# Kernel optimization log

Measured on AMD Instinct MI355X. Metric: run time of the kernel, lower is better.

## Reference

```python
import jax, jax.numpy as jnp
import numpy as np

TEMPERATURE = 0.5
EPS = 1e-8  # torch cosine_similarity norm clamp


def setup_inputs() -> dict:
    key = jax.random.key(0)
    k1, k2, k3 = jax.random.split(key, 3)
    N, D = 4096, 256
    z_i = jax.random.normal(k1, (N, D), dtype=jnp.float32)
    z_j = jax.random.normal(k2, (N, D), dtype=jnp.float32)
    weights = jax.random.uniform(k3, (N,), dtype=jnp.float32)
    return {"z_i": z_i, "z_j": z_j, "weights": weights}


def reference(z_i, z_j, weights):
    N = z_i.shape[0]
    z = jnp.concatenate([z_i, z_j], axis=0)  # [2N, D]
    # cosine similarity via normalized matmul (same math as broadcasted F.cosine_similarity)
    norm = jnp.maximum(jnp.linalg.norm(z, axis=1, keepdims=True), EPS)
    zn = z / norm
    sim = zn @ zn.T  # [2N, 2N]
    # positives: diagonals at offsets +N and -N
    sim_ij = jnp.diagonal(sim, offset=N)
    sim_ji = jnp.diagonal(sim, offset=-N)
    positives = jnp.concatenate([sim_ij, sim_ji], axis=0)  # [2N]
    mask = 1.0 - jnp.eye(2 * N, dtype=sim.dtype)
    denominator = jnp.sum(mask * jnp.exp(sim / TEMPERATURE), axis=1)  # [2N]
    numerator = jnp.exp(positives / TEMPERATURE)
    all_losses = -jnp.log(numerator / denominator)  # [2N]
    w2 = jnp.tile(weights, 2)  # weights.repeat(2)
    loss = jnp.sum(all_losses * w2) / jnp.sum(w2)
    return loss
```

## Files before the change

### kernel.cpp

```cpp
#include <hip/hip_runtime.h>
#include <hip/hip_bf16.h>

#define PN   4096
#define PN2  8192
#define PD   256
#define TILE 128
#define BK   64
#define NBLK (PN2 / TILE)
#define NTRI (NBLK * (NBLK + 1) / 2)

typedef __attribute__((ext_vector_type(8))) short bf16x8;
typedef __attribute__((ext_vector_type(4))) float f32x4;

typedef const __attribute__((address_space(1))) void* gas_ptr;
typedef __attribute__((address_space(3))) void* las_ptr;

__global__ __launch_bounds__(256) void normalize_kernel(
    const float* __restrict__ zi, const float* __restrict__ zj,
    __hip_bfloat16* __restrict__ zn, float* __restrict__ rowsum) {
  int r = blockIdx.x;
  int tid = threadIdx.x;
  const float* src = (r < PN) ? (zi + (size_t)r * PD) : (zj + (size_t)(r - PN) * PD);
  float x = src[tid];
  float s = x * x;
  #pragma unroll
  for (int off = 32; off >= 1; off >>= 1) s += __shfl_xor(s, off, 64);
  __shared__ float p[4];
  if ((tid & 63) == 0) p[tid >> 6] = s;
  __syncthreads();
  float tot = p[0] + p[1] + p[2] + p[3];
  float nrm = fmaxf(sqrtf(tot), 1e-8f);
  zn[(size_t)r * PD + tid] = __float2bfloat16(x / nrm);
  if (tid == 0) rowsum[r] = 0.0f;
}

__global__ __launch_bounds__(256) void simsum_kernel(
    const __hip_bfloat16* __restrict__ zn,
    float* __restrict__ rowsum, float* __restrict__ pos) {
  __shared__ char lds[2 * TILE * BK * 2];
  char* As = lds;
  char* Bs = lds + TILE * BK * 2;

  const int idx = blockIdx.x;
  int bj = (int)((sqrtf(8.0f * (float)idx + 1.0f) - 1.0f) * 0.5f);
  while ((bj + 1) * (bj + 2) / 2 <= idx) ++bj;
  while (bj * (bj + 1) / 2 > idx) --bj;
  const int bi = idx - bj * (bj + 1) / 2;
  const bool diagBlk = (bi == bj);
  const bool posBlk  = (bj == bi + PN / TILE);

  const int tid  = threadIdx.x;
  const int wave = tid >> 6;
  const int lane = tid & 63;
  const int quad = lane >> 4;
  const int c16  = lane & 15;
  const int rowBase = bi * TILE;
  const int colBase = bj * TILE;
  const int waveRow = (wave >> 1) * 64;
  const int waveCol = (wave & 1) * 64;

  f32x4 acc[4][4];
  #pragma unroll
  for (int i = 0; i < 4; ++i)
    #pragma unroll
    for (int j = 0; j < 4; ++j)
      acc[i][j] = (f32x4){0.f, 0.f, 0.f, 0.f};

  const int subrow = lane >> 3;
  const int slot   = lane & 7;
  const char* BsEff = diagBlk ? As : Bs;

  for (int kt = 0; kt < PD / BK; ++kt) {
    if (kt) __syncthreads();
    #pragma unroll
    for (int p = 0; p < 4; ++p) {
      int issue = wave * 4 + p;
      int r = issue * 8 + subrow;
      int c = slot ^ (r & 7);
      const __hip_bfloat16* ga = zn + (size_t)(rowBase + r) * PD + kt * BK + c * 8;
      __builtin_amdgcn_global_load_lds((gas_ptr)ga, (las_ptr)(As + issue * 1024), 16, 0, 0);
      if (!diagBlk) {
        const __hip_bfloat16* gb = zn + (size_t)(colBase + r) * PD + kt * BK + c * 8;
        __builtin_amdgcn_global_load_lds((gas_ptr)gb, (las_ptr)(Bs + issue * 1024), 16, 0, 0);
      }
    }
    __syncthreads();

    #pragma unroll
    for (int ki = 0; ki < 2; ++ki) {
      bf16x8 a[4], b[4];
      #pragma unroll
      for (int mi = 0; mi < 4; ++mi) {
        int r = waveRow + mi * 16 + c16;
        int ch = quad + ki * 4;
        a[mi] = *(const bf16x8*)(As + r * 128 + ((ch ^ (r & 7)) * 16));
      }
      #pragma unroll
      for (int ni = 0; ni < 4; ++ni) {
        int r = waveCol + ni * 16 + c16;
        int ch = quad + ki * 4;
        b[ni] = *(const bf16x8*)(BsEff + r * 128 + ((ch ^ (r & 7)) * 16));
      }
      #pragma unroll
      for (int mi = 0; mi < 4; ++mi)
        #pragma unroll
        for (int ni = 0; ni < 4; ++ni)
          acc[mi][ni] = __builtin_amdgcn_mfma_f32_16x16x32_bf16(a[mi], b[ni], acc[mi][ni], 0, 0, 0);
    }
  }

  float colsum[4] = {0.f, 0.f, 0.f, 0.f};
  #pragma unroll
  for (int mi = 0; mi < 4; ++mi) {
    int rbase = rowBase + waveRow + mi * 16 + quad * 4;
    float rs[4] = {0.f, 0.f, 0.f, 0.f};
    #pragma unroll
    for (int ni = 0; ni < 4; ++ni) {
      int gcol = colBase + waveCol + ni * 16 + c16;
      #pragma unroll
      for (int t = 0; t < 4; ++t) {
        int grow = rbase + t;
        float sim = acc[mi][ni][t];
        float e = __expf(2.0f * sim);
        if (diagBlk && gcol == grow) e = 0.0f;
        rs[t] += e;
        colsum[ni] += e;
        if (posBlk && gcol == grow + PN) {
          pos[grow] = sim;
          pos[grow + PN] = sim;
        }
      }
    }
    #pragma unroll
    for (int t = 0; t < 4; ++t) {
      #pragma unroll
      for (int off = 1; off <= 8; off <<= 1) rs[t] += __shfl_xor(rs[t], off, 64);
    }
    if (c16 == 0) {
      #pragma unroll
      for (int t = 0; t < 4; ++t) atomicAdd(&rowsum[rbase + t], rs[t]);
    }
  }
  if (!diagBlk) {
    #pragma unroll
    for (int ni = 0; ni < 4; ++ni) {
      float cs = colsum[ni];
      cs += __shfl_xor(cs, 16, 64);
      cs += __shfl_xor(cs, 32, 64);
      if (quad == 0) atomicAdd(&rowsum[colBase + waveCol + ni * 16 + c16], cs);
    }
  }
}

__global__ __launch_bounds__(1024) void finalize_kernel(
    const float* __restrict__ rowsum, const float* __restrict__ pos,
    const float* __restrict__ w, float* __restrict__ out) {
  int tid = threadIdx.x;
  float wl = 0.f, ws = 0.f;
  for (int i = tid; i < PN2; i += 1024) {
    float li = logf(rowsum[i]) - 2.0f * pos[i];
    float wi = w[i & (PN - 1)];
    wl += wi * li;
    ws += wi;
  }
  #pragma unroll
  for (int off = 32; off >= 1; off >>= 1) {
    wl += __shfl_xor(wl, off, 64);
    ws += __shfl_xor(ws, off, 64);
  }
  __shared__ float pl[16], pw[16];
  if ((tid & 63) == 0) { pl[tid >> 6] = wl; pw[tid >> 6] = ws; }
  __syncthreads();
  if (tid == 0) {
    float sl = 0.f, sw = 0.f;
    #pragma unroll
    for (int k = 0; k < 16; ++k) { sl += pl[k]; sw += pw[k]; }
    out[0] = sl / sw;
  }
}

extern "C" void kernel_launch(void* const* d_in, const int* in_sizes, int n_in,
                              void* d_out, int out_size, void* d_ws, size_t ws_size,
                              hipStream_t stream) {
  const float* zi = (const float*)d_in[0];
  const float* zj = (const float*)d_in[1];
  const float* w  = (const float*)d_in[2];
  float* out = (float*)d_out;

  __hip_bfloat16* zn = (__hip_bfloat16*)d_ws;
  float* rowsum = (float*)((char*)d_ws + (size_t)PN2 * PD * 2);
  float* pos = rowsum + PN2;

  normalize_kernel<<<PN2, 256, 0, stream>>>(zi, zj, zn, rowsum);
  simsum_kernel<<<NTRI, 256, 0, stream>>>(zn, rowsum, pos);
  finalize_kernel<<<1, 1024, 0, stream>>>(rowsum, pos, w, out);
}
```

Baseline: 110.7 us.

## Load MFMA operands directly from global memory and vectorize normalization per wave

The similarity kernel no longer stages tiles in LDS with global_load_lds and barriers. Each lane now loads its bf16x8 MFMA fragments straight from global memory into registers, double-buffered across the eight K-steps. This removes LDS traffic and __syncthreads, but every wave re-reads rows that other waves in the block share, so it relies on L1/L2 cache hits. The normalize kernel is also changed to one wave per row with float4 loads and packed bf16 stores, which drops the shared-memory reduction.

```diff
diff --git a/kernel.cpp b/kernel.cpp
--- a/kernel.cpp
+++ b/kernel.cpp
@@ -5,42 +5,36 @@
 #define PN2  8192
 #define PD   256
 #define TILE 128
-#define BK   64
 #define NBLK (PN2 / TILE)
 #define NTRI (NBLK * (NBLK + 1) / 2)
 
 typedef __attribute__((ext_vector_type(8))) short bf16x8;
 typedef __attribute__((ext_vector_type(4))) float f32x4;
 
-typedef const __attribute__((address_space(1))) void* gas_ptr;
-typedef __attribute__((address_space(3))) void* las_ptr;
-
 __global__ __launch_bounds__(256) void normalize_kernel(
     const float* __restrict__ zi, const float* __restrict__ zj,
     __hip_bfloat16* __restrict__ zn, float* __restrict__ rowsum) {
-  int r = blockIdx.x;
-  int tid = threadIdx.x;
+  const int wave = threadIdx.x >> 6;
+  const int lane = threadIdx.x & 63;
+  const int r = blockIdx.x * 4 + wave;
   const float* src = (r < PN) ? (zi + (size_t)r * PD) : (zj + (size_t)(r - PN) * PD);
-  float x = src[tid];
-  float s = x * x;
+  float4 x = *(const float4*)(src + lane * 4);
+  float s = x.x * x.x + x.y * x.y + x.z * x.z + x.w * x.w;
   #pragma unroll
   for (int off = 32; off >= 1; off >>= 1) s += __shfl_xor(s, off, 64);
-  __shared__ float p[4];
-  if ((tid & 63) == 0) p[tid >> 6] = s;
-  __syncthreads();
-  float tot = p[0] + p[1] + p[2] + p[3];
-  float nrm = fmaxf(sqrtf(tot), 1e-8f);
-  zn[(size_t)r * PD + tid] = __float2bfloat16(x / nrm);
-  if (tid == 0) rowsum[r] = 0.0f;
+  float inv = 1.0f / fmaxf(sqrtf(s), 1e-8f);
+  union { ushort4 u; __hip_bfloat16 h[4]; } o;
+  o.h[0] = __float2bfloat16(x.x * inv);
+  o.h[1] = __float2bfloat16(x.y * inv);
+  o.h[2] = __float2bfloat16(x.z * inv);
+  o.h[3] = __float2bfloat16(x.w * inv);
+  *(ushort4*)((unsigned short*)zn + (size_t)r * PD + lane * 4) = o.u;
+  if (lane == 0) rowsum[r] = 0.0f;
 }
 
 __global__ __launch_bounds__(256) void simsum_kernel(
     const __hip_bfloat16* __restrict__ zn,
     float* __restrict__ rowsum, float* __restrict__ pos) {
-  __shared__ char lds[2 * TILE * BK * 2];
-  char* As = lds;
-  char* Bs = lds + TILE * BK * 2;
-
   const int idx = blockIdx.x;
   int bj = (int)((sqrtf(8.0f * (float)idx + 1.0f) - 1.0f) * 0.5f);
   while ((bj + 1) * (bj + 2) / 2 <= idx) ++bj;
@@ -59,6 +53,10 @@
   const int waveRow = (wave >> 1) * 64;
   const int waveCol = (wave & 1) * 64;
 
+  const unsigned short* zs = (const unsigned short*)zn;
+  const unsigned short* baseA = zs + (size_t)(rowBase + waveRow + c16) * PD + quad * 8;
+  const unsigned short* baseB = zs + (size_t)(colBase + waveCol + c16) * PD + quad * 8;
+
   f32x4 acc[4][4];
   #pragma unroll
   for (int i = 0; i < 4; ++i)
@@ -66,47 +64,29 @@
     for (int j = 0; j < 4; ++j)
       acc[i][j] = (f32x4){0.f, 0.f, 0.f, 0.f};
 
-  const int subrow = lane >> 3;
-  const int slot   = lane & 7;
-  const char* BsEff = diagBlk ? As : Bs;
-
-  for (int kt = 0; kt < PD / BK; ++kt) {
-    if (kt) __syncthreads();
-    #pragma unroll
-    for (int p = 0; p < 4; ++p) {
-      int issue = wave * 4 + p;
-      int r = issue * 8 + subrow;
-      int c = slot ^ (r & 7);
-      const __hip_bfloat16* ga = zn + (size_t)(rowBase + r) * PD + kt * BK + c * 8;
-      __builtin_amdgcn_global_load_lds((gas_ptr)ga, (las_ptr)(As + issue * 1024), 16, 0, 0);
-      if (!diagBlk) {
-        const __hip_bfloat16* gb = zn + (size_t)(colBase + r) * PD + kt * BK + c * 8;
-        __builtin_amdgcn_global_load_lds((gas_ptr)gb, (las_ptr)(Bs + issue * 1024), 16, 0, 0);
+  bf16x8 abuf[2][4], bbuf[2][4];
+  #pragma unroll
+  for (int mi = 0; mi < 4; ++mi) {
+    abuf[0][mi] = *(const bf16x8*)(baseA + mi * 16 * PD);
+    bbuf[0][mi] = *(const bf16x8*)(baseB + mi * 16 * PD);
+  }
+  #pragma unroll
+  for (int ks = 0; ks < PD / 32; ++ks) {
+    const int cur = ks & 1;
+    const int nxt = cur ^ 1;
+    if (ks < PD / 32 - 1) {
+      #pragma unroll
+      for (int mi = 0; mi < 4; ++mi) {
+        abuf[nxt][mi] = *(const bf16x8*)(baseA + mi * 16 * PD + (ks + 1) * 32);
+        bbuf[nxt][mi] = *(const bf16x8*)(baseB + mi * 16 * PD + (ks + 1) * 32);
       }
     }
-    __syncthreads();
-
     #pragma unroll
-    for (int ki = 0; ki < 2; ++ki) {
-      bf16x8 a[4], b[4];
+    for (int mi = 0; mi < 4; ++mi)
       #pragma unroll
-      for (int mi = 0; mi < 4; ++mi) {
-        int r = waveRow + mi * 16 + c16;
-        int ch = quad + ki * 4;
-        a[mi] = *(const bf16x8*)(As + r * 128 + ((ch ^ (r & 7)) * 16));
-      }
-      #pragma unroll
-      for (int ni = 0; ni < 4; ++ni) {
-        int r = waveCol + ni * 16 + c16;
-        int ch = quad + ki * 4;
-        b[ni] = *(const bf16x8*)(BsEff + r * 128 + ((ch ^ (r & 7)) * 16));
-      }
-      #pragma unroll
-      for (int mi = 0; mi < 4; ++mi)
-        #pragma unroll
-        for (int ni = 0; ni < 4; ++ni)
-          acc[mi][ni] = __builtin_amdgcn_mfma_f32_16x16x32_bf16(a[mi], b[ni], acc[mi][ni], 0, 0, 0);
-    }
+      for (int ni = 0; ni < 4; ++ni)
+        acc[mi][ni] = __builtin_amdgcn_mfma_f32_16x16x32_bf16(
+            abuf[cur][mi], bbuf[cur][ni], acc[mi][ni], 0, 0, 0);
   }
 
   float colsum[4] = {0.f, 0.f, 0.f, 0.f};
@@ -191,7 +171,7 @@
   float* rowsum = (float*)((char*)d_ws + (size_t)PN2 * PD * 2);
   float* pos = rowsum + PN2;
 
-  normalize_kernel<<<PN2, 256, 0, stream>>>(zi, zj, zn, rowsum);
+  normalize_kernel<<<PN2 / 4, 256, 0, stream>>>(zi, zj, zn, rowsum);
   simsum_kernel<<<NTRI, 256, 0, stream>>>(zn, rowsum, pos);
   finalize_kernel<<<1, 1024, 0, stream>>>(rowsum, pos, w, out);
 }
```

Result: slower. 151.5 us (+36.8%).

## Replace global row-sum atomics with per-tile partials and a parallel finalize

Applied to the files above, without the earlier changes.

The similarity kernel now gathers row and column exp-sums in shared memory and writes one partial per tile-row into a [NBLK x 2N] buffer, instead of issuing global atomics. Finalize runs across 32 blocks, reduces those partials, and uses a ticket counter so the last block writes the loss. Normalize now uses one wave per row with float4 loads, and the block index is remapped to spread the triangular tiles across the grid. This removes global atomic contention and the single-block finalize, but adds a larger workspace and an extra pass over the partial buffer.

```diff
diff --git a/kernel.cpp b/kernel.cpp
--- a/kernel.cpp
+++ b/kernel.cpp
@@ -17,31 +17,42 @@
 
 __global__ __launch_bounds__(256) void normalize_kernel(
     const float* __restrict__ zi, const float* __restrict__ zj,
-    __hip_bfloat16* __restrict__ zn, float* __restrict__ rowsum) {
-  int r = blockIdx.x;
-  int tid = threadIdx.x;
+    __hip_bfloat16* __restrict__ zn, float* __restrict__ wlws,
+    unsigned* __restrict__ ticket) {
+  const int wave = threadIdx.x >> 6;
+  const int lane = threadIdx.x & 63;
+  const int r = blockIdx.x * 4 + wave;
   const float* src = (r < PN) ? (zi + (size_t)r * PD) : (zj + (size_t)(r - PN) * PD);
-  float x = src[tid];
-  float s = x * x;
+  float4 x = *(const float4*)(src + lane * 4);
+  float s = x.x * x.x + x.y * x.y + x.z * x.z + x.w * x.w;
   #pragma unroll
   for (int off = 32; off >= 1; off >>= 1) s += __shfl_xor(s, off, 64);
-  __shared__ float p[4];
-  if ((tid & 63) == 0) p[tid >> 6] = s;
-  __syncthreads();
-  float tot = p[0] + p[1] + p[2] + p[3];
-  float nrm = fmaxf(sqrtf(tot), 1e-8f);
-  zn[(size_t)r * PD + tid] = __float2bfloat16(x / nrm);
-  if (tid == 0) rowsum[r] = 0.0f;
+  float inv = 1.0f / fmaxf(sqrtf(s), 1e-8f);
+  union { ushort4 u; __hip_bfloat16 h[4]; } o;
+  o.h[0] = __float2bfloat16(x.x * inv);
+  o.h[1] = __float2bfloat16(x.y * inv);
+  o.h[2] = __float2bfloat16(x.z * inv);
+  o.h[3] = __float2bfloat16(x.w * inv);
+  *(ushort4*)((unsigned short*)zn + (size_t)r * PD + lane * 4) = o.u;
+  if (r == 0) {
+    if (lane == 0) { wlws[0] = 0.0f; wlws[1] = 0.0f; }
+    if (lane == 1) *ticket = 0u;
+  }
 }
 
 __global__ __launch_bounds__(256) void simsum_kernel(
     const __hip_bfloat16* __restrict__ zn,
-    float* __restrict__ rowsum, float* __restrict__ pos) {
+    float* __restrict__ rowpart, float* __restrict__ pos) {
   __shared__ char lds[2 * TILE * BK * 2];
+  __shared__ float rowacc[TILE];
+  __shared__ float colacc[TILE];
   char* As = lds;
   char* Bs = lds + TILE * BK * 2;
 
-  const int idx = blockIdx.x;
+  const int tid  = threadIdx.x;
+  if (tid < TILE) { rowacc[tid] = 0.0f; colacc[tid] = 0.0f; }
+
+  const int idx = (int)((blockIdx.x & 7) * (NTRI / 8) + (blockIdx.x >> 3));
   int bj = (int)((sqrtf(8.0f * (float)idx + 1.0f) - 1.0f) * 0.5f);
   while ((bj + 1) * (bj + 2) / 2 <= idx) ++bj;
   while (bj * (bj + 1) / 2 > idx) --bj;
@@ -49,7 +60,6 @@
   const bool diagBlk = (bi == bj);
   const bool posBlk  = (bj == bi + PN / TILE);
 
-  const int tid  = threadIdx.x;
   const int wave = tid >> 6;
   const int lane = tid & 63;
   const int quad = lane >> 4;
@@ -112,14 +122,14 @@
   float colsum[4] = {0.f, 0.f, 0.f, 0.f};
   #pragma unroll
   for (int mi = 0; mi < 4; ++mi) {
-    int rbase = rowBase + waveRow + mi * 16 + quad * 4;
+    int lrow = waveRow + mi * 16 + quad * 4;
     float rs[4] = {0.f, 0.f, 0.f, 0.f};
     #pragma unroll
     for (int ni = 0; ni < 4; ++ni) {
       int gcol = colBase + waveCol + ni * 16 + c16;
       #pragma unroll
       for (int t = 0; t < 4; ++t) {
-        int grow = rbase + t;
+        int grow = rowBase + lrow + t;
         float sim = acc[mi][ni][t];
         float e = __expf(2.0f * sim);
         if (diagBlk && gcol == grow) e = 0.0f;
@@ -138,7 +148,7 @@
     }
     if (c16 == 0) {
       #pragma unroll
-      for (int t = 0; t < 4; ++t) atomicAdd(&rowsum[rbase + t], rs[t]);
+      for (int t = 0; t < 4; ++t) atomicAdd(&rowacc[lrow + t], rs[t]);
     }
   }
   if (!diagBlk) {
@@ -147,35 +157,48 @@
       float cs = colsum[ni];
       cs += __shfl_xor(cs, 16, 64);
       cs += __shfl_xor(cs, 32, 64);
-      if (quad == 0) atomicAdd(&rowsum[colBase + waveCol + ni * 16 + c16], cs);
-    }
-  }
-}
-
-__global__ __launch_bounds__(1024) void finalize_kernel(
-    const float* __restrict__ rowsum, const float* __restrict__ pos,
-    const float* __restrict__ w, float* __restrict__ out) {
-  int tid = threadIdx.x;
-  float wl = 0.f, ws = 0.f;
-  for (int i = tid; i < PN2; i += 1024) {
-    float li = logf(rowsum[i]) - 2.0f * pos[i];
-    float wi = w[i & (PN - 1)];
-    wl += wi * li;
-    ws += wi;
-  }
+      if (quad == 0) atomicAdd(&colacc[waveCol + ni * 16 + c16], cs);
+    }
+  }
+
+  __syncthreads();
+  if (tid < TILE) {
+    rowpart[(size_t)bj * PN2 + rowBase + tid] = rowacc[tid];
+    if (!diagBlk)
+      rowpart[(size_t)bi * PN2 + colBase + tid] = colacc[tid];
+  }
+}
+
+__global__ __launch_bounds__(256) void finalize_kernel(
+    const float* __restrict__ rowpart, const float* __restrict__ pos,
+    const float* __restrict__ w, float* __restrict__ wlws,
+    unsigned* __restrict__ ticket, float* __restrict__ out) {
+  const int tid = threadIdx.x;
+  const int r = blockIdx.x * 256 + tid;
+  float s = 0.0f;
+  #pragma unroll 8
+  for (int x = 0; x < NBLK; ++x) s += rowpart[(size_t)x * PN2 + r];
+  float li = logf(s) - 2.0f * pos[r];
+  float wi = w[r & (PN - 1)];
+  float wl = wi * li, ws = wi;
   #pragma unroll
   for (int off = 32; off >= 1; off >>= 1) {
     wl += __shfl_xor(wl, off, 64);
     ws += __shfl_xor(ws, off, 64);
   }
-  __shared__ float pl[16], pw[16];
-  if ((tid & 63) == 0) { pl[tid >> 6] = wl; pw[tid >> 6] = ws; }
+  __shared__ float pl[4], pw[4];
+  const int lane = tid & 63, wv = tid >> 6;
+  if (lane == 0) { pl[wv] = wl; pw[wv] = ws; }
   __syncthreads();
   if (tid == 0) {
-    float sl = 0.f, sw = 0.f;
-    #pragma unroll
-    for (int k = 0; k < 16; ++k) { sl += pl[k]; sw += pw[k]; }
-    out[0] = sl / sw;
+    atomicAdd(&wlws[0], pl[0] + pl[1] + pl[2] + pl[3]);
+    atomicAdd(&wlws[1], pw[0] + pw[1] + pw[2] + pw[3]);
+    __threadfence();
+    if (atomicAdd(ticket, 1u) == 31) {
+      float a = atomicAdd(&wlws[0], 0.0f);
+      float b = atomicAdd(&wlws[1], 0.0f);
+      out[0] = a / b;
+    }
   }
 }
 
@@ -188,10 +211,12 @@
   float* out = (float*)d_out;
 
   __hip_bfloat16* zn = (__hip_bfloat16*)d_ws;
-  float* rowsum = (float*)((char*)d_ws + (size_t)PN2 * PD * 2);
-  float* pos = rowsum + PN2;
-
-  normalize_kernel<<<PN2, 256, 0, stream>>>(zi, zj, zn, rowsum);
-  simsum_kernel<<<NTRI, 256, 0, stream>>>(zn, rowsum, pos);
-  finalize_kernel<<<1, 1024, 0, stream>>>(rowsum, pos, w, out);
-}
+  float* rowpart = (float*)((char*)d_ws + (size_t)PN2 * PD * 2);
+  float* pos     = rowpart + (size_t)NBLK * PN2;
+  float* wlws    = pos + PN2;
+  unsigned* ticket = (unsigned*)(wlws + 2);
+
+  normalize_kernel<<<PN2 / 4, 256, 0, stream>>>(zi, zj, zn, wlws, ticket);
+  simsum_kernel<<<NTRI, 256, 0, stream>>>(zn, rowpart, pos);
+  finalize_kernel<<<32, 256, 0, stream>>>(rowpart, pos, w, wlws, ticket, out);
+}
```

Measured after the change: 109.1 us. About the same (-1.4%).
